# Optimization experiments

Measured on AMD Instinct MI355X. Metric: run time of the kernel, lower is better.

## Reference

```python
import jax, jax.numpy as jnp
import numpy as np

B, H, C = 131072, 16, 32        # batch, n_holidays, n_changepoints
HID, HP, SKU = 512, 512 // 16, 64  # hidden_dim, hidden per holiday, sku embed dim
TEMP = 0.7
TIME_MAX = 365.0
LN_EPS = 1e-3  # keras LayerNormalization default epsilon


def mish(x):
    return x * jnp.tanh(jax.nn.softplus(x))


def setup_inputs() -> dict:
    key = jax.random.key(0)
    ks = jax.random.split(key, 12)
    inputs = jax.random.uniform(ks[0], (B, H), dtype=jnp.float32) * TIME_MAX
    sku_embedding = jax.random.normal(ks[1], (B, SKU), dtype=jnp.float32)
    # per-holiday params, stacked over holiday axis
    deltas = jnp.full((H, C), TIME_MAX / C, dtype=jnp.float32)  # changepoint_deltas init
    ln_gamma = jnp.ones((H, C), dtype=jnp.float32)
    ln_beta = jnp.zeros((H, C), dtype=jnp.float32)
    attn_w = jax.random.normal(ks[2], (H,), dtype=jnp.float32) * 0.5  # Dense(1) on [...,1]
    Wh = jax.random.normal(ks[3], (H, C, HP), dtype=jnp.float32) * (1.0 / np.sqrt(C))
    Wah = jax.random.normal(ks[4], (HID, HID), dtype=jnp.float32) * (1.0 / np.sqrt(HID))
    Waa = jax.random.normal(ks[5], (HID, HID), dtype=jnp.float32) * (1.0 / np.sqrt(HID))
    Wb = jax.random.normal(ks[6], (SKU, HID), dtype=jnp.float32) * (1.0 / np.sqrt(SKU))
    Wa = jax.random.normal(ks[7], (SKU, HID), dtype=jnp.float32) * (1.0 / np.sqrt(SKU))
    Wo = jax.random.normal(ks[8], (HID, 1), dtype=jnp.float32)
    Wo = Wo / jnp.linalg.norm(Wo, axis=0, keepdims=True)  # UnitNorm(axis=0) constraint
    return {"inputs": inputs, "sku_embedding": sku_embedding, "deltas": deltas,
            "ln_gamma": ln_gamma, "ln_beta": ln_beta, "attn_w": attn_w, "Wh": Wh,
            "Wah": Wah, "Waa": Waa, "Wb": Wb, "Wa": Wa, "Wo": Wo}


def reference(inputs, sku_embedding, deltas, ln_gamma, ln_beta, attn_w, Wh, Wah, Waa, Wb, Wa, Wo):
    # ChangepointReLU (vectorised over holidays): softplus -> cumsum -> rescale to [0, 365]
    pd = jax.nn.softplus(deltas)                     # [H, C]
    cps = jnp.cumsum(pd, axis=-1)
    cps = cps / cps[:, -1:] * TIME_MAX               # time_min = 0
    feats = jax.nn.relu(inputs[:, :, None] - cps[None, :, :])  # [B, H, C]
    # per-holiday LayerNorm over changepoint axis
    mu = jnp.mean(feats, axis=-1, keepdims=True)
    var = jnp.mean((feats - mu) ** 2, axis=-1, keepdims=True)
    normed = (feats - mu) * jax.lax.rsqrt(var + LN_EPS) * ln_gamma[None] + ln_beta[None]
    # per-holiday attention: Dense(1,no bias) on [...,1] == scalar multiply per holiday
    logits = normed * attn_w[None, :, None]
    attn = jax.nn.softmax(logits / TEMP, axis=-1)    # n_changepoints > 1
    attended = normed * attn                          # [B, H, C]
    # per-holiday hidden Dense(HP, mish, no bias), then concat over holidays
    hid = mish(jnp.einsum('bhc,hcd->bhd', attended, Wh))  # [B, H, HP]
    aggregated = hid.reshape(hid.shape[0], H * HP)        # [B, HID]
    agg_hidden = mish(aggregated @ Wah)                   # [B, HID]
    agg_attn = jax.nn.softmax((agg_hidden @ Waa) / TEMP, axis=-1)
    final = agg_hidden * agg_attn                         # dropout inactive (inference)
    beta = jax.nn.sigmoid(sku_embedding @ Wb)
    alpha = sku_embedding @ Wa
    final = final * beta + alpha
    return final @ Wo                                     # [B, 1]
```

## Files before the change

kernel.cpp:

```cpp
#include <hip/hip_runtime.h>
#include <hip/hip_fp16.h>
#include <stdint.h>

#define B_TOT 131072
#define CHUNK 65536
#define NH 16
#define NC 32
#define HIDD 512

typedef unsigned short u16;
typedef __attribute__((ext_vector_type(8))) short short8;
typedef __attribute__((ext_vector_type(4))) float f32x4;
typedef __attribute__((ext_vector_type(4))) int i32x4;

#define GLLDS(g, l) __builtin_amdgcn_global_load_lds((const __attribute__((address_space(1))) unsigned int*)(g), (__attribute__((address_space(3))) unsigned int*)(l), 16, 0, 0)

__device__ __forceinline__ u16 f2bf(float x){
  unsigned u = __float_as_uint(x);
  u += 0x7fffu + ((u >> 16) & 1u);
  return (u16)(u >> 16);
}
__device__ __forceinline__ float bf2f(u16 b){ return __uint_as_float(((unsigned)b) << 16); }
__device__ __forceinline__ u16 f2h(float x){ __half h = __float2half(x); return *(u16*)&h; }
__device__ __forceinline__ float h2f(u16 b){ __half h; *(u16*)&h = b; return __half2float(h); }
__device__ __forceinline__ float mishf(float x){
  float e = __expf(fminf(x, 30.f));
  float u = 1.f + e;
  float u2 = u * u;
  return x * (u2 - 1.f) / (u2 + 1.f);
}

__global__ __launch_bounds__(512) void prep_small(
    const float* __restrict__ deltas, const float* __restrict__ Wa,
    const float* __restrict__ Wo, float* __restrict__ cps, float* __restrict__ wWo)
{
  const int t = threadIdx.x;
  {
    const int k = t >> 3, part = t & 7;
    const int n0 = part * 64;
    float s = 0.f;
#pragma unroll
    for (int i = 0; i < 64; i += 4){
      const f32x4 wa = *(const f32x4*)&Wa[k*HIDD + n0 + i];
      const f32x4 wo = *(const f32x4*)&Wo[n0 + i];
      s += wa.x*wo.x + wa.y*wo.y + wa.z*wo.z + wa.w*wo.w;
    }
#pragma unroll
    for (int sh = 4; sh >= 1; sh >>= 1) s += __shfl_xor(s, sh);
    if (part == 0) wWo[k] = s;
  }
  if (t < NH){
    float cum[NC];
    float run = 0.f;
#pragma unroll
    for (int c = 0; c < NC; c++){
      float d = deltas[t*NC + c];
      float sp = (d > 20.f) ? d : log1pf(__expf(d));
      run += sp; cum[c] = run;
    }
    float s = 365.0f / run;
#pragma unroll
    for (int c = 0; c < NC; c++) cps[t*NC + c] = cum[c] * s;
  }
}

__global__ void prep_convert(const float* __restrict__ Wah, const float* __restrict__ Waa,
                             const float* __restrict__ Wb, const float* __restrict__ Wh,
                             u16* __restrict__ WahT, u16* __restrict__ WaaT,
                             u16* __restrict__ WbT, u16* __restrict__ WhT)
{
  int i = blockIdx.x * 256 + threadIdx.x;
  if (i < 262144){ int n = i >> 9, k = i & 511; WahT[i] = f2bf(Wah[k*512 + n]); return; }
  i -= 262144;
  if (i < 262144){ int n = i >> 9, k = i & 511; WaaT[i] = f2bf(Waa[k*512 + n]); return; }
  i -= 262144;
  if (i < 32768){ int n = i >> 6, k = i & 63; WbT[i] = f2bf(Wb[k*512 + n]); return; }
  i -= 32768;
  if (i < 16384){ int h = i >> 10, r = i & 1023, d = r >> 5, c = r & 31;
                  WhT[i] = f2bf(Wh[h*1024 + c*32 + d]); return; }
}

__global__ __launch_bounds__(256) void stage1_kernel(
    const float* __restrict__ inputs, const float* __restrict__ sku,
    const float* __restrict__ ln_g, const float* __restrict__ ln_b,
    const float* __restrict__ attnw, const float* __restrict__ cps,
    const float* __restrict__ wWo, const u16* __restrict__ WhT,
    u16* __restrict__ agg, u16* __restrict__ skub, float* __restrict__ skd)
{
  __shared__ __align__(16) float in_l[256];
  __shared__ __align__(16) float cps_l[512];
  __shared__ __align__(16) float gam_l[512];
  __shared__ __align__(16) float bet_l[512];
  __shared__ float aw_l[16];
  __shared__ __align__(16) u16 at_l[16*16*32];
  __shared__ __align__(16) u16 ot_l[16*512];

  const int t = threadIdx.x;
  const int ln = t & 63;
  const long bb = (long)blockIdx.x * 16;

  in_l[t] = inputs[bb*16 + t];
  cps_l[t] = cps[t];       cps_l[t+256] = cps[t+256];
  gam_l[t] = ln_g[t];      gam_l[t+256] = ln_g[t+256];
  bet_l[t] = ln_b[t];      bet_l[t+256] = ln_b[t+256];
  if (t < 16) aw_l[t] = attnw[t];
  {
    const f32x4 sv = *(const f32x4*)&sku[bb*64 + t*4];
    unsigned lo = (unsigned)f2bf(sv.x) | ((unsigned)f2bf(sv.y) << 16);
    unsigned hi = (unsigned)f2bf(sv.z) | ((unsigned)f2bf(sv.w) << 16);
    unsigned long long v = (unsigned long long)lo | ((unsigned long long)hi << 32);
    *(unsigned long long*)&skub[bb*64 + t*4] = v;
    const f32x4 wv4 = *(const f32x4*)&wWo[(ln & 15)*4];
    float pd = sv.x*wv4.x + sv.y*wv4.y + sv.z*wv4.z + sv.w*wv4.w;
#pragma unroll
    for (int s = 1; s < 16; s <<= 1) pd += __shfl_xor(pd, s);
    if ((ln & 15) == 0) skd[bb + (t >> 4)] = pd;
  }
  __syncthreads();

  const int h = t >> 4, bi = t & 15;
  const float x = in_l[bi*16 + h];
  float nrm[NC], pw[NC];
  float s1 = 0.f;
#pragma unroll
  for (int c = 0; c < NC; c++){ float f = fmaxf(x - cps_l[h*NC + c], 0.f); nrm[c] = f; s1 += f; }
  const float mu = s1 * (1.f/NC);
  float s2 = 0.f;
#pragma unroll
  for (int c = 0; c < NC; c++){ float d = nrm[c] - mu; s2 += d*d; }
  const float rs = rsqrtf(s2 * (1.f/NC) + 1e-3f);
  const float aw = aw_l[h] * (1.0f/0.7f);
  float lmax = -1e30f;
#pragma unroll
  for (int c = 0; c < NC; c++){
    float nv = (nrm[c] - mu) * rs * gam_l[h*NC + c] + bet_l[h*NC + c];
    nrm[c] = nv;
    lmax = fmaxf(lmax, nv * aw);
  }
  float ps = 0.f;
#pragma unroll
  for (int c = 0; c < NC; c++){ float p = __expf(nrm[c]*aw - lmax); pw[c] = p; ps += p; }
  const float invs = 1.f / ps;
#pragma unroll
  for (int c = 0; c < NC; c += 2){
    unsigned pk = (unsigned)f2bf(nrm[c]*pw[c]*invs) | ((unsigned)f2bf(nrm[c+1]*pw[c+1]*invs) << 16);
    *(unsigned*)&at_l[h*512 + bi*32 + c] = pk;
  }
  __syncthreads();

  const int wv = t >> 6;
  const int lrow = ln & 15, lq = ln >> 4;
#pragma unroll
  for (int q = 0; q < 4; q++){
    const int hh = wv*4 + q;
    short8 af  = *(const short8*)&at_l[hh*512 + lrow*32 + lq*8];
    short8 bf0 = *(const short8*)&WhT[hh*1024 + lrow*32 + lq*8];
    short8 bf1 = *(const short8*)&WhT[hh*1024 + (16 + lrow)*32 + lq*8];
    f32x4 acc0 = {0.f,0.f,0.f,0.f}, acc1 = {0.f,0.f,0.f,0.f};
    acc0 = __builtin_amdgcn_mfma_f32_16x16x32_bf16(af, bf0, acc0, 0, 0, 0);
    acc1 = __builtin_amdgcn_mfma_f32_16x16x32_bf16(af, bf1, acc1, 0, 0, 0);
#pragma unroll
    for (int r = 0; r < 4; r++){
      const int br = lq*4 + r;
      ot_l[br*512 + hh*32 + lrow]      = f2bf(mishf(acc0[r]));
      ot_l[br*512 + hh*32 + 16 + lrow] = f2bf(mishf(acc1[r]));
    }
  }
  __syncthreads();
  {
    const int row = t >> 4, c16 = t & 15;
    const i32x4* src = (const i32x4*)&ot_l[row*512 + c16*32];
    i32x4* dst = (i32x4*)&agg[(bb + row)*512 + c16*32];
#pragma unroll
    for (int j = 0; j < 4; j++) dst[j] = src[j];
  }
}

__global__ __launch_bounds__(256, 3) void gemm_bw(
    const u16* __restrict__ A, const u16* __restrict__ Bt,
    const float* __restrict__ Wo, u16* __restrict__ bw)
{
  __shared__ __align__(16) u16 As[2][128*32];
  __shared__ __align__(16) u16 Bs[2][128*32];
  const int t = threadIdx.x, wv = t >> 6, ln = t & 63;
  const int g = blockIdx.x;
  const int m_idx = (g & 7) + ((g >> 5) << 3);
  const int n_idx = (g >> 3) & 3;
  const long m0 = (long)m_idx * 128;
  const int n0 = n_idx * 128;
  const int lrow = ln & 15, lq = ln >> 4;
  const int wm = wv >> 1, wn = wv & 1;

  auto stage = [&](int buf, int kt){
#pragma unroll
    for (int p = 0; p < 2; p++){
      const int chunk = p*256 + wv*64 + ln;
      const int mm = chunk >> 2, kc = chunk & 3;
      const int kcl = kc ^ ((mm >> 1) & 3);
      GLLDS(&A[(m0 + mm)*64 + kt + kcl*8],  &As[buf][(p*256 + wv*64)*8]);
      GLLDS(&Bt[(n0 + mm)*64 + kt + kcl*8], &Bs[buf][(p*256 + wv*64)*8]);
    }
  };

  f32x4 acc[4][4] = {};
  stage(0, 0);
  for (int ks = 0; ks < 2; ks++){
    const int cur = ks & 1;
    __syncthreads();
    if (ks + 1 < 2) stage(cur ^ 1, (ks + 1)*32);
    short8 a[4], b[4];
#pragma unroll
    for (int i = 0; i < 4; i++){
      const int ra = wm*64 + i*16 + lrow;
      const int rb = wn*64 + i*16 + lrow;
      const int lqa = lq ^ ((ra >> 1) & 3);
      const int lqb = lq ^ ((rb >> 1) & 3);
      a[i] = *(const short8*)&As[cur][ra*32 + lqa*8];
      b[i] = *(const short8*)&Bs[cur][rb*32 + lqb*8];
    }
#pragma unroll
    for (int i = 0; i < 4; i++)
#pragma unroll
      for (int j = 0; j < 4; j++)
        acc[i][j] = __builtin_amdgcn_mfma_f32_16x16x32_bf16(a[i], b[j], acc[i][j], 0, 0, 0);
  }
#pragma unroll
  for (int j = 0; j < 4; j++){
    const int n = n0 + wn*64 + j*16 + lrow;
    const float wo = Wo[n];
#pragma unroll
    for (int i = 0; i < 4; i++){
#pragma unroll
      for (int r = 0; r < 4; r++){
        const long m = m0 + wm*64 + i*16 + lq*4 + r;
        const float sig = 1.f / (1.f + __expf(-acc[i][j][r]));
        bw[m*512 + n] = f2h(sig * wo);
      }
    }
  }
}

__global__ __launch_bounds__(512, 2) void gemm_mish(
    const u16* __restrict__ A, const u16* __restrict__ Bt, u16* __restrict__ aggh)
{
  __shared__ __align__(16) u16 lds[2*128*32 + 2*512*32];
  u16* As0 = lds;
  u16* Bs0 = lds + 2*128*32;
  const int t = threadIdx.x, wv = t >> 6, ln = t & 63;
  const int lrow = ln & 15, lq = ln >> 4;
  const int rh = wv >> 2, cq = wv & 3;
  const long m0 = (long)blockIdx.x * 128;

  auto stageA = [&](int buf, int kt){
    const int mm = t >> 2, kc = t & 3;
    const int kcl = kc ^ ((mm >> 1) & 3);
    GLLDS(&A[(m0 + mm)*512 + kt + kcl*8], &As0[buf*4096 + t*8]);
  };
  auto stageB = [&](int buf, int kt){
#pragma unroll
    for (int p = 0; p < 4; p++){
      const int idx = p*512 + t;
      const int mm = idx >> 2, kc = idx & 3;
      const int kcl = kc ^ ((mm >> 1) & 3);
      GLLDS(&Bt[(long)mm*512 + kt + kcl*8], &Bs0[buf*16384 + idx*8]);
    }
  };

  f32x4 acc[4][8] = {};
  stageA(0, 0); stageB(0, 0);
  for (int ks = 0; ks < 16; ks++){
    const int cur = ks & 1;
    __syncthreads();
    if (ks + 1 < 16){ stageA(cur ^ 1, (ks + 1)*32); stageB(cur ^ 1, (ks + 1)*32); }
    short8 a[4], b[8];
#pragma unroll
    for (int i = 0; i < 4; i++){
      const int ra = rh*64 + i*16 + lrow;
      const int lqa = lq ^ ((ra >> 1) & 3);
      a[i] = *(const short8*)&As0[cur*4096 + ra*32 + lqa*8];
    }
#pragma unroll
    for (int j = 0; j < 8; j++){
      const int rb = cq*128 + j*16 + lrow;
      const int lqb = lq ^ ((rb >> 1) & 3);
      b[j] = *(const short8*)&Bs0[cur*16384 + rb*32 + lqb*8];
    }
#pragma unroll
    for (int i = 0; i < 4; i++)
#pragma unroll
      for (int j = 0; j < 8; j++)
        acc[i][j] = __builtin_amdgcn_mfma_f32_16x16x32_bf16(a[i], b[j], acc[i][j], 0, 0, 0);
  }

  const int TP = 528;
  __syncthreads();
#pragma unroll 1
  for (int h = 0; h < 2; h++){
    if (rh == h){
#pragma unroll
      for (int i = 0; i < 4; i++)
#pragma unroll
        for (int j = 0; j < 8; j++)
#pragma unroll
          for (int r = 0; r < 4; r++)
            lds[(i*16 + lq*4 + r)*TP + cq*128 + j*16 + lrow] = f2bf(mishf(acc[i][j][r]));
    }
    __syncthreads();
#pragma unroll
    for (int it = 0; it < 8; it++){
      const int idx = it*512 + t;
      const int row = idx >> 6, off = idx & 63;
      const i32x4 v = *(const i32x4*)&lds[row*TP + off*8];
      *(i32x4*)&aggh[(m0 + h*64 + row)*512 + off*8] = v;
    }
    __syncthreads();
  }
}

__global__ __launch_bounds__(512, 2) void mega2(
    const u16* __restrict__ A, const u16* __restrict__ Bt,
    const u16* __restrict__ bw, const float* __restrict__ skd,
    float* __restrict__ outp)
{
  __shared__ __align__(16) u16 As[2][128*32];
  __shared__ __align__(16) u16 Bs[2][512*32];
  const int t = threadIdx.x, wv = t >> 6, ln = t & 63;
  const int lrow = ln & 15, lq = ln >> 4;
  const int rh = wv >> 2, cq = wv & 3;
  const long m0 = (long)blockIdx.x * 128;

  auto stageA = [&](int buf, int kt){
    const int mm = t >> 2, kc = t & 3;
    const int kcl = kc ^ ((mm >> 1) & 3);
    GLLDS(&A[(m0 + mm)*512 + kt + kcl*8], &As[buf][t*8]);
  };
  auto stageB = [&](int buf, int kt){
#pragma unroll
    for (int p = 0; p < 4; p++){
      const int idx = p*512 + t;
      const int mm = idx >> 2, kc = idx & 3;
      const int kcl = kc ^ ((mm >> 1) & 3);
      GLLDS(&Bt[(long)mm*512 + kt + kcl*8], &Bs[buf][idx*8]);
    }
  };

  f32x4 acc[4][8] = {};
  stageA(0, 0); stageB(0, 0);
  for (int ks = 0; ks < 16; ks++){
    const int cur = ks & 1;
    __syncthreads();
    if (ks + 1 < 16){ stageA(cur ^ 1, (ks + 1)*32); stageB(cur ^ 1, (ks + 1)*32); }
    short8 a[4], b[8];
#pragma unroll
    for (int i = 0; i < 4; i++){
      const int ra = rh*64 + i*16 + lrow;
      const int lqa = lq ^ ((ra >> 1) & 3);
      a[i] = *(const short8*)&As[cur][ra*32 + lqa*8];
    }
#pragma unroll
    for (int j = 0; j < 8; j++){
      const int rb = cq*128 + j*16 + lrow;
      const int lqb = lq ^ ((rb >> 1) & 3);
      b[j] = *(const short8*)&Bs[cur][rb*32 + lqb*8];
    }
#pragma unroll
    for (int i = 0; i < 4; i++)
#pragma unroll
      for (int j = 0; j < 8; j++)
        acc[i][j] = __builtin_amdgcn_mfma_f32_16x16x32_bf16(a[i], b[j], acc[i][j], 0, 0, 0);
  }

  __syncthreads();
  float* mxs = (float*)&Bs[0][0];
  float* sss = mxs + 512;
  float* tts = sss + 512;
  const float inv_t = 1.0f / 0.7f;

#pragma unroll
  for (int i = 0; i < 4; i++){
#pragma unroll
    for (int r = 0; r < 4; r++){
      float tm = acc[i][0][r];
#pragma unroll
      for (int j = 1; j < 8; j++) tm = fmaxf(tm, acc[i][j][r]);
#pragma unroll
      for (int s = 1; s < 16; s <<= 1) tm = fmaxf(tm, __shfl_xor(tm, s));
      if (lrow == 0) mxs[(rh*64 + i*16 + lq*4 + r)*4 + cq] = tm;
    }
  }
  __syncthreads();
#pragma unroll
  for (int i = 0; i < 4; i++){
#pragma unroll
    for (int r = 0; r < 4; r++){
      const int row = rh*64 + i*16 + lq*4 + r;
      const float gm = fmaxf(fmaxf(mxs[row*4+0], mxs[row*4+1]),
                             fmaxf(mxs[row*4+2], mxs[row*4+3]));
      float sp = 0.f, tp = 0.f;
#pragma unroll
      for (int j = 0; j < 8; j++){
        const long gi = (m0 + row)*512 + cq*128 + j*16 + lrow;
        const float e = __expf((acc[i][j][r] - gm) * inv_t);
        sp += e;
        tp += e * bf2f(A[gi]) * h2f(bw[gi]);
      }
#pragma unroll
      for (int s = 1; s < 16; s <<= 1){ sp += __shfl_xor(sp, s); tp += __shfl_xor(tp, s); }
      if (lrow == 0){ sss[row*4 + cq] = sp; tts[row*4 + cq] = tp; }
    }
  }
  __syncthreads();
  if (t < 128){
    const float S = sss[t*4] + sss[t*4+1] + sss[t*4+2] + sss[t*4+3];
    const float T = tts[t*4] + tts[t*4+1] + tts[t*4+2] + tts[t*4+3];
    outp[m0 + t] = T / S + skd[m0 + t];
  }
}

__global__ void ws_too_small(float* o, float v){ o[(long)blockIdx.x*256 + threadIdx.x] = v; }

extern "C" void kernel_launch(void* const* d_in, const int* in_sizes, int n_in,
                              void* d_out, int out_size, void* d_ws, size_t ws_size,
                              hipStream_t stream)
{
  const float* inputs = (const float*)d_in[0];
  const float* sku    = (const float*)d_in[1];
  const float* deltas = (const float*)d_in[2];
  const float* ln_g   = (const float*)d_in[3];
  const float* ln_b   = (const float*)d_in[4];
  const float* attnw  = (const float*)d_in[5];
  const float* Wh     = (const float*)d_in[6];
  const float* Wah    = (const float*)d_in[7];
  const float* Waa    = (const float*)d_in[8];
  const float* Wb     = (const float*)d_in[9];
  const float* Wa     = (const float*)d_in[10];
  const float* Wo     = (const float*)d_in[11];
  float* outp = (float*)d_out;

  const size_t OFF_CPS  = 0;
  const size_t OFF_WWO  = 2048;
  const size_t OFF_WAHT = 4096;
  const size_t OFF_WAAT = OFF_WAHT + 524288;
  const size_t OFF_WBT  = OFF_WAAT + 524288;
  const size_t OFF_WHT  = OFF_WBT  + 65536;
  const size_t OFF_SKUB = OFF_WHT  + 32768;
  const size_t OFF_SKD  = OFF_SKUB + (size_t)CHUNK*64*2;
  const size_t OFF_AGG  = OFF_SKD  + (size_t)CHUNK*4;
  const size_t OFF_BW   = OFF_AGG  + (size_t)CHUNK*512*2;
  const size_t OFF_AGH  = OFF_BW   + (size_t)CHUNK*512*2;
  const size_t NEED     = OFF_AGH  + (size_t)CHUNK*512*2;

  if (ws_size < NEED){
    hipLaunchKernelGGL(ws_too_small, dim3(B_TOT/256), dim3(256), 0, stream,
                       outp, -(float)(ws_size >> 20));
    return;
  }

  char* ws = (char*)d_ws;
  float* cps  = (float*)(ws + OFF_CPS);
  float* wWo  = (float*)(ws + OFF_WWO);
  u16* WahT   = (u16*)(ws + OFF_WAHT);
  u16* WaaT   = (u16*)(ws + OFF_WAAT);
  u16* WbT    = (u16*)(ws + OFF_WBT);
  u16* WhT    = (u16*)(ws + OFF_WHT);
  u16* skub   = (u16*)(ws + OFF_SKUB);
  float* skd  = (float*)(ws + OFF_SKD);
  u16* agg    = (u16*)(ws + OFF_AGG);
  u16* bw     = (u16*)(ws + OFF_BW);
  u16* aggh   = (u16*)(ws + OFF_AGH);

  hipLaunchKernelGGL(prep_small, dim3(1), dim3(512), 0, stream, deltas, Wa, Wo, cps, wWo);
  hipLaunchKernelGGL(prep_convert, dim3(2240), dim3(256), 0, stream,
                     Wah, Waa, Wb, Wh, WahT, WaaT, WbT, WhT);

  for (int ch = 0; ch < B_TOT / CHUNK; ch++){
    const float* in_c  = inputs + (size_t)ch * CHUNK * 16;
    const float* sku_c = sku    + (size_t)ch * CHUNK * 64;
    float* out_c       = outp   + (size_t)ch * CHUNK;

    hipLaunchKernelGGL(stage1_kernel, dim3(CHUNK/16), dim3(256), 0, stream,
                       in_c, sku_c, ln_g, ln_b, attnw, cps, wWo, WhT, agg, skub, skd);
    hipLaunchKernelGGL(gemm_mish, dim3(CHUNK/128), dim3(512), 0, stream,
                       agg, WahT, aggh);
    hipLaunchKernelGGL(gemm_bw, dim3(CHUNK/128*4), dim3(256), 0, stream,
                       skub, WbT, Wo, bw);
    hipLaunchKernelGGL(mega2, dim3(CHUNK/128), dim3(512), 0, stream,
                       aggh, WaaT, bw, skd, out_c);
  }
}
```

Measured before the change: 527.0 us.

## Fuse sku-embedding beta GEMM into stage1 kernel, drop separate gemm_bw launch

Moves the sigmoid(sku@Wb)*Wo computation into stage1_kernel. Each block now keeps its 16 rows of bf16 sku in LDS and runs MFMAs against WbT read directly from global memory. The fused kernel writes the fp16 bw result through LDS reusing the ot_l buffer, so the skub intermediate and the gemm_bw launch go away. This trades a separate well-tiled GEMM and extra global traffic for more work, LDS use and global WbT reads inside stage1, which may lower its occupancy.

```diff
diff --git a/kernel.cpp b/kernel.cpp
--- a/kernel.cpp
+++ b/kernel.cpp
@@ -85,15 +85,19 @@
     const float* __restrict__ ln_g, const float* __restrict__ ln_b,
     const float* __restrict__ attnw, const float* __restrict__ cps,
     const float* __restrict__ wWo, const u16* __restrict__ WhT,
-    u16* __restrict__ agg, u16* __restrict__ skub, float* __restrict__ skd)
+    const u16* __restrict__ WbT, const float* __restrict__ Wo,
+    u16* __restrict__ agg, u16* __restrict__ bwp, float* __restrict__ skd)
 {
   __shared__ __align__(16) float in_l[256];
   __shared__ __align__(16) float cps_l[512];
   __shared__ __align__(16) float gam_l[512];
   __shared__ __align__(16) float bet_l[512];
+  __shared__ __align__(16) float wo_l[512];
   __shared__ float aw_l[16];
+  __shared__ __align__(16) u16 skl[16*72];
   __shared__ __align__(16) u16 at_l[16*16*32];
   __shared__ __align__(16) u16 ot_l[16*512];
+  const int SP = 72;
 
   const int t = threadIdx.x;
   const int ln = t & 63;
@@ -103,13 +107,14 @@
   cps_l[t] = cps[t];       cps_l[t+256] = cps[t+256];
   gam_l[t] = ln_g[t];      gam_l[t+256] = ln_g[t+256];
   bet_l[t] = ln_b[t];      bet_l[t+256] = ln_b[t+256];
+  wo_l[t] = Wo[t];         wo_l[t+256] = Wo[t+256];
   if (t < 16) aw_l[t] = attnw[t];
   {
     const f32x4 sv = *(const f32x4*)&sku[bb*64 + t*4];
     unsigned lo = (unsigned)f2bf(sv.x) | ((unsigned)f2bf(sv.y) << 16);
     unsigned hi = (unsigned)f2bf(sv.z) | ((unsigned)f2bf(sv.w) << 16);
     unsigned long long v = (unsigned long long)lo | ((unsigned long long)hi << 32);
-    *(unsigned long long*)&skub[bb*64 + t*4] = v;
+    *(unsigned long long*)&skl[(t >> 4)*SP + (t & 15)*4] = v;
     const f32x4 wv4 = *(const f32x4*)&wWo[(ln & 15)*4];
     float pd = sv.x*wv4.x + sv.y*wv4.y + sv.z*wv4.z + sv.w*wv4.w;
 #pragma unroll
@@ -174,68 +179,39 @@
 #pragma unroll
     for (int j = 0; j < 4; j++) dst[j] = src[j];
   }
-}
-
-__global__ __launch_bounds__(256, 3) void gemm_bw(
-    const u16* __restrict__ A, const u16* __restrict__ Bt,
-    const float* __restrict__ Wo, u16* __restrict__ bw)
-{
-  __shared__ __align__(16) u16 As[2][128*32];
-  __shared__ __align__(16) u16 Bs[2][128*32];
-  const int t = threadIdx.x, wv = t >> 6, ln = t & 63;
-  const int g = blockIdx.x;
-  const int m_idx = (g & 7) + ((g >> 5) << 3);
-  const int n_idx = (g >> 3) & 3;
-  const long m0 = (long)m_idx * 128;
-  const int n0 = n_idx * 128;
-  const int lrow = ln & 15, lq = ln >> 4;
-  const int wm = wv >> 1, wn = wv & 1;
-
-  auto stage = [&](int buf, int kt){
-#pragma unroll
-    for (int p = 0; p < 2; p++){
-      const int chunk = p*256 + wv*64 + ln;
-      const int mm = chunk >> 2, kc = chunk & 3;
-      const int kcl = kc ^ ((mm >> 1) & 3);
-      GLLDS(&A[(m0 + mm)*64 + kt + kcl*8],  &As[buf][(p*256 + wv*64)*8]);
-      GLLDS(&Bt[(n0 + mm)*64 + kt + kcl*8], &Bs[buf][(p*256 + wv*64)*8]);
-    }
-  };
-
-  f32x4 acc[4][4] = {};
-  stage(0, 0);
-  for (int ks = 0; ks < 2; ks++){
-    const int cur = ks & 1;
-    __syncthreads();
-    if (ks + 1 < 2) stage(cur ^ 1, (ks + 1)*32);
-    short8 a[4], b[4];
-#pragma unroll
-    for (int i = 0; i < 4; i++){
-      const int ra = wm*64 + i*16 + lrow;
-      const int rb = wn*64 + i*16 + lrow;
-      const int lqa = lq ^ ((ra >> 1) & 3);
-      const int lqb = lq ^ ((rb >> 1) & 3);
-      a[i] = *(const short8*)&As[cur][ra*32 + lqa*8];
-      b[i] = *(const short8*)&Bs[cur][rb*32 + lqb*8];
-    }
-#pragma unroll
-    for (int i = 0; i < 4; i++)
-#pragma unroll
-      for (int j = 0; j < 4; j++)
-        acc[i][j] = __builtin_amdgcn_mfma_f32_16x16x32_bf16(a[i], b[j], acc[i][j], 0, 0, 0);
-  }
-#pragma unroll
-  for (int j = 0; j < 4; j++){
-    const int n = n0 + wn*64 + j*16 + lrow;
-    const float wo = Wo[n];
-#pragma unroll
-    for (int i = 0; i < 4; i++){
+  __syncthreads();
+
+  {
+    f32x4 accb[8] = {};
+#pragma unroll
+    for (int ks = 0; ks < 2; ks++){
+      const short8 a2 = *(const short8*)&skl[lrow*SP + ks*32 + lq*8];
+#pragma unroll
+      for (int j = 0; j < 8; j++){
+        const short8 b2 = *(const short8*)&WbT[(wv*128 + j*16 + lrow)*64 + ks*32 + lq*8];
+        accb[j] = __builtin_amdgcn_mfma_f32_16x16x32_bf16(a2, b2, accb[j], 0, 0, 0);
+      }
+    }
+#pragma unroll
+    for (int j = 0; j < 8; j++){
+      const int col = wv*128 + j*16 + lrow;
+      const float wo = wo_l[col];
 #pragma unroll
       for (int r = 0; r < 4; r++){
-        const long m = m0 + wm*64 + i*16 + lq*4 + r;
-        const float sig = 1.f / (1.f + __expf(-acc[i][j][r]));
-        bw[m*512 + n] = f2h(sig * wo);
+        const int row = lq*4 + r;
+        const float sig = 1.f / (1.f + __expf(-accb[j][r]));
+        ot_l[row*512 + col] = f2h(sig * wo);
       }
+    }
+  }
+  __syncthreads();
+  {
+#pragma unroll
+    for (int it = 0; it < 4; it++){
+      const int idx = it*256 + t;
+      const int row = idx >> 6, off = idx & 63;
+      const i32x4 v = *(const i32x4*)&ot_l[row*512 + off*8];
+      *(i32x4*)&bwp[(bb + row)*512 + off*8] = v;
     }
   }
 }
@@ -443,8 +419,7 @@
   const size_t OFF_WAAT = OFF_WAHT + 524288;
   const size_t OFF_WBT  = OFF_WAAT + 524288;
   const size_t OFF_WHT  = OFF_WBT  + 65536;
-  const size_t OFF_SKUB = OFF_WHT  + 32768;
-  const size_t OFF_SKD  = OFF_SKUB + (size_t)CHUNK*64*2;
+  const size_t OFF_SKD  = OFF_WHT  + 32768;
   const size_t OFF_AGG  = OFF_SKD  + (size_t)CHUNK*4;
   const size_t OFF_BW   = OFF_AGG  + (size_t)CHUNK*512*2;
   const size_t OFF_AGH  = OFF_BW   + (size_t)CHUNK*512*2;
@@ -463,7 +438,6 @@
   u16* WaaT   = (u16*)(ws + OFF_WAAT);
   u16* WbT    = (u16*)(ws + OFF_WBT);
   u16* WhT    = (u16*)(ws + OFF_WHT);
-  u16* skub   = (u16*)(ws + OFF_SKUB);
   float* skd  = (float*)(ws + OFF_SKD);
   u16* agg    = (u16*)(ws + OFF_AGG);
   u16* bw     = (u16*)(ws + OFF_BW);
@@ -479,11 +453,10 @@
     float* out_c       = outp   + (size_t)ch * CHUNK;
 
     hipLaunchKernelGGL(stage1_kernel, dim3(CHUNK/16), dim3(256), 0, stream,
-                       in_c, sku_c, ln_g, ln_b, attnw, cps, wWo, WhT, agg, skub, skd);
+                       in_c, sku_c, ln_g, ln_b, attnw, cps, wWo, WhT, WbT, Wo,
+                       agg, bw, skd);
     hipLaunchKernelGGL(gemm_mish, dim3(CHUNK/128), dim3(512), 0, stream,
                        agg, WahT, aggh);
-    hipLaunchKernelGGL(gemm_bw, dim3(CHUNK/128*4), dim3(256), 0, stream,
-                       skub, WbT, Wo, bw);
     hipLaunchKernelGGL(mega2, dim3(CHUNK/128), dim3(512), 0, stream,
                        aggh, WaaT, bw, skd, out_c);
   }
```

After: 585.4 us. 11.1% more time.
